# Optimization experiments

Measured on AMD Instinct MI355X. Metric: run time of the kernel, lower is better.

Reference implementation:

```python
import jax, jax.numpy as jnp
import numpy as np

B, POMO, N = 64, 200, 1000
EMB, H, D = 128, 8, 16  # head_num * qkv_dim == embedding_dim
SQRT_EMB = 11.313708498984761
CLIP = 10.0
LORA_SCALE = 16.0 / 16  # alpha / rank = 1.0


def setup_inputs() -> dict:
    key = jax.random.key(0)
    ks = jax.random.split(key, 12)
    s = 1.0 / np.sqrt(EMB)
    return {
        "encoded_nodes": jax.random.normal(ks[0], (B, N, EMB), jnp.float32),
        "encoded_q1": jax.random.normal(ks[1], (B, POMO, EMB), jnp.float32),
        "encoded_last_node": jax.random.normal(ks[2], (B, POMO, EMB), jnp.float32),
        "ninf_mask": jnp.zeros((B, POMO, N), jnp.float32),
        "Wq_first": jax.random.normal(ks[3], (H * D, EMB), jnp.float32) * s,
        "Wq_last": jax.random.normal(ks[4], (H * D, EMB), jnp.float32) * s,
        "Wk": jax.random.normal(ks[5], (H * D, EMB), jnp.float32) * s,
        "Wv": jax.random.normal(ks[6], (H * D, EMB), jnp.float32) * s,
        "Wcomb": jax.random.normal(ks[7], (EMB, H * D), jnp.float32) * s,
        "bcomb": jnp.zeros((EMB,), jnp.float32),
        "lora_q_A": jax.random.normal(ks[8], (16, EMB), jnp.float32) * s,
        "lora_q_B": jax.random.normal(ks[9], (H * D, 16), jnp.float32) * 0.01,
        "lora_c_A": jax.random.normal(ks[10], (16, H * D), jnp.float32) * s,
        "lora_c_B": jax.random.normal(ks[11], (EMB, 16), jnp.float32) * 0.01,
    }


def _heads(x):
    # [B, n, H*D] -> [B, H, n, D]
    b, n, _ = x.shape
    return x.reshape(b, n, H, D).transpose(0, 2, 1, 3)


def reference(encoded_nodes, encoded_q1, encoded_last_node, ninf_mask,
              Wq_first, Wq_last, Wk, Wv, Wcomb, bcomb,
              lora_q_A, lora_q_B, lora_c_A, lora_c_B):
    # set_kv
    k = _heads(encoded_nodes @ Wk.T)   # [B,H,N,D]
    v = _heads(encoded_nodes @ Wv.T)   # [B,H,N,D]
    # set_q1
    q_first = _heads(encoded_q1 @ Wq_first.T)  # [B,H,POMO,D]
    # forward: Wq_last + LoRA delta
    q_last_lin = encoded_last_node @ Wq_last.T \
        + ((encoded_last_node @ lora_q_A.T) @ lora_q_B.T) * LORA_SCALE
    q = q_first + _heads(q_last_lin)  # [B,H,POMO,D]
    # masked multi-head attention (rank3 mask broadcast over heads)
    score = jnp.einsum('bhnd,bhmd->bhnm', q, k) / jnp.sqrt(jnp.float32(D))
    score = score + ninf_mask[:, None, :, :]
    weights = jax.nn.softmax(score, axis=3)
    out = jnp.einsum('bhnm,bhmd->bhnd', weights, v)  # [B,H,POMO,D]
    out_concat = out.transpose(0, 2, 1, 3).reshape(encoded_q1.shape[0], -1, H * D)
    # combine + LoRA delta
    mh = out_concat @ Wcomb.T + bcomb \
        + ((out_concat @ lora_c_A.T) @ lora_c_B.T) * LORA_SCALE  # [B,POMO,EMB]
    # single-head scoring against encoder embeddings, tanh clip, mask, softmax
    score2 = jnp.einsum('bne,bme->bnm', mh, encoded_nodes) / SQRT_EMB
    score_masked = CLIP * jnp.tanh(score2) + ninf_mask
    probs = jax.nn.softmax(score_masked, axis=2)  # [B,POMO,N]
    return probs
```

## Files before the change

### kernel.cpp

```cpp
#include <hip/hip_runtime.h>
#include <hip/hip_bf16.h>


typedef _Float16 f16;
typedef _Float16 f16x2 __attribute__((ext_vector_type(2)));
typedef _Float16 f16x4 __attribute__((ext_vector_type(4)));
typedef _Float16 f16x8 __attribute__((ext_vector_type(8)));
typedef __fp16  h4   __attribute__((ext_vector_type(4)));
typedef float   f32x4 __attribute__((ext_vector_type(4)));

#define LORA_SCALE 1.0f
#define L2E 1.44269504f

__device__ __forceinline__ f16x2 pk2(f16 a, f16 b){ f16x2 r; r[0]=a; r[1]=b; return r; }

#if __has_builtin(__builtin_amdgcn_fdot2)
__device__ __forceinline__ float fdot2f(f16x2 a, f16x2 b, float c){ return __builtin_amdgcn_fdot2(a, b, c, false); }
#else
__device__ __forceinline__ float fdot2f(f16x2 a, f16x2 b, float c){ return c + (float)a[0]*(float)b[0] + (float)a[1]*(float)b[1]; }
#endif

#if __has_builtin(__builtin_amdgcn_cvt_pkrtz)
__device__ __forceinline__ f16x2 pkrtz(float a, float b){
  return __builtin_bit_cast(f16x2, __builtin_amdgcn_cvt_pkrtz(a, b));
}
#else
__device__ __forceinline__ f16x2 pkrtz(float a, float b){ return pk2((f16)a, (f16)b); }
#endif

__device__ __forceinline__ f32x4 mfma16(f16x4 a, f16x4 b, f32x4 c){
  return __builtin_amdgcn_mfma_f32_16x16x16f16(
      __builtin_bit_cast(h4, a), __builtin_bit_cast(h4, b), c, 0, 0, 0);
}

__device__ __forceinline__ float sumsq16(const f16* p){
  const f16x8* v = (const f16x8*)p;
  f16x8 a = v[0], b = v[1];
  float s = 0.f;
  s = fdot2f(pk2(a[0],a[1]), pk2(a[0],a[1]), s);
  s = fdot2f(pk2(a[2],a[3]), pk2(a[2],a[3]), s);
  s = fdot2f(pk2(a[4],a[5]), pk2(a[4],a[5]), s);
  s = fdot2f(pk2(a[6],a[7]), pk2(a[6],a[7]), s);
  s = fdot2f(pk2(b[0],b[1]), pk2(b[0],b[1]), s);
  s = fdot2f(pk2(b[2],b[3]), pk2(b[2],b[3]), s);
  s = fdot2f(pk2(b[4],b[5]), pk2(b[4],b[5]), s);
  s = fdot2f(pk2(b[6],b[7]), pk2(b[6],b[7]), s);
  return s;
}

__global__ __launch_bounds__(256) void k0_wconv(const float* __restrict__ Wk,
    const float* __restrict__ Wv, f16* __restrict__ WkvF)
{
  const int i = blockIdx.x*256 + threadIdx.x;
  const float4 v = (i < 4096) ? ((const float4*)Wk)[i] : ((const float4*)Wv)[i-4096];
  f16x2 lo = pkrtz(v.x,v.y), hi = pkrtz(v.z,v.w);
  f16x4 o = __builtin_shufflevector(lo, hi, 0, 1, 2, 3);
  *(f16x4*)(WkvF + i*4) = o;
}

#define NSTR 132
#define WSTR 136
__global__ __launch_bounds__(256) void k1_proj(const float* __restrict__ nodes,
    const f16* __restrict__ WkvF,
    f16* __restrict__ nodesT, f16* __restrict__ Kp, f16* __restrict__ Vt)
{
  __shared__ f16 lds[64*NSTR];
  __shared__ f16 wlds[16*WSTR];
  const int tid = threadIdx.x, lane = tid & 63, w = tid >> 6;
  const int b = blockIdx.y;
  const int n0 = blockIdx.x * 64;
  const int rows = min(64, 1000 - n0);
  for (int i = tid; i < rows*32; i += 256) {
    const int r = i >> 5, cq = i & 31;
    float4 v = ((const float4*)(nodes + ((size_t)b*1000 + n0 + r)*128))[cq];
    f16x2 lo = pkrtz(v.x,v.y), hi = pkrtz(v.z,v.w);
    f16x4 o = __builtin_shufflevector(lo, hi, 0, 1, 2, 3);
    *(f16x4*)(lds + r*NSTR + cq*4) = o;
    const int grow = n0 + r;
    const int t = grow >> 4, gcol = grow & 15;
    const int kk = cq >> 2, gg = cq & 3;
    f16* dstT = nodesT + (((size_t)(b*63 + t)*8 + kk)*256);
    *(f16x4*)(dstT + (gg*16 + gcol)*4) = o;
    if (grow == 999) {
      f16* d62 = nodesT + (((size_t)(b*63 + 62)*8 + kk)*256);
      #pragma unroll
      for (int cf = 8; cf < 16; ++cf) *(f16x4*)(d62 + (gg*16 + cf)*4) = o;
    }
  }
  __syncthreads();
  const int col = lane & 15, g = lane >> 4, g4 = g*4;
  const int mloc = w*16 + col;
  f16x4 nf[8];
  #pragma unroll
  for (int kk = 0; kk < 8; ++kk)
    nf[kk] = *(const f16x4*)(lds + min(mloc, rows-1)*NSTR + kk*16 + g4);
  const int wr = tid >> 4, wc = tid & 15;
  for (int ct = 0; ct < 16; ++ct) {
    __syncthreads();
    *(f16x8*)(wlds + wr*WSTR + wc*8) =
        *(const f16x8*)(WkvF + (ct*16 + wr)*128 + wc*8);
    __syncthreads();
    f16x4 wf[8];
    #pragma unroll
    for (int kk = 0; kk < 8; ++kk)
      wf[kk] = *(const f16x4*)(wlds + col*WSTR + kk*16 + g4);
    f32x4 acc = {0.f, 0.f, 0.f, 0.f};
    if (ct < 8) {
      #pragma unroll
      for (int kk = 0; kk < 8; ++kk) acc = mfma16(wf[kk], nf[kk], acc);
      if (mloc < rows) {
        const int nn = n0 + mloc;
        f16x4 ov = __builtin_shufflevector(pk2((f16)acc[0],(f16)acc[1]),
                                           pk2((f16)acc[2],(f16)acc[3]), 0,1,2,3);
        *(f16x4*)(Kp + ((size_t)(b*8+ct)*1000 + nn)*16 + g4) = ov;
      }
    } else {
      #pragma unroll
      for (int kk = 0; kk < 8; ++kk) acc = mfma16(nf[kk], wf[kk], acc);
      if (w*16 + g4 + 3 < rows) {
        const int nbase = n0 + w*16 + g4;
        f16x4 ov = __builtin_shufflevector(pk2((f16)acc[0],(f16)acc[1]),
                                           pk2((f16)acc[2],(f16)acc[3]), 0,1,2,3);
        *(f16x4*)(Vt + ((size_t)(b*8+(ct-8))*16 + col)*1000 + nbase) = ov;
      }
    }
  }
}

__global__ __launch_bounds__(256) void k1b_kmax(const f16* __restrict__ Kp,
    float* __restrict__ kmaxA)
{
  __shared__ float wmax[4];
  const int bh = blockIdx.x, tid = threadIdx.x, lane = tid & 63, w = tid >> 6;
  const f16* base = Kp + (size_t)bh*16000;
  float mx = 0.f;
  for (int n = tid; n < 1000; n += 256) mx = fmaxf(mx, sumsq16(base + n*16));
  #pragma unroll
  for (int off = 32; off; off >>= 1) mx = fmaxf(mx, __shfl_xor(mx, off, 64));
  if (lane == 0) wmax[w] = mx;
  __syncthreads();
  if (tid == 0) {
    float m = fmaxf(fmaxf(wmax[0], wmax[1]), fmaxf(wmax[2], wmax[3]));
    kmaxA[bh] = sqrtf(m);
  }
}

__global__ __launch_bounds__(256) void k2_q(const float* __restrict__ q1,
    const float* __restrict__ last, const float* __restrict__ Wqf,
    const float* __restrict__ Wql, const float* __restrict__ lqA,
    const float* __restrict__ lqB, f16* __restrict__ qF)
{
  __shared__ f16 q1r[32*128];
  __shared__ f16 lar[32*128];
  __shared__ float t16[32*16];
  const int tid = threadIdx.x;
  const int row0 = blockIdx.x * 32;
  {
    const float4* s1 = (const float4*)(q1 + (size_t)row0*128);
    const float4* s2 = (const float4*)(last + (size_t)row0*128);
    f16x2* d1 = (f16x2*)q1r; f16x2* d2 = (f16x2*)lar;
    for (int i = tid; i < 32*32; i += 256) {
      float4 v = s1[i];
      d1[2*i] = pkrtz(v.x,v.y); d1[2*i+1] = pkrtz(v.z,v.w);
      float4 u = s2[i];
      d2[2*i] = pkrtz(u.x,u.y); d2[2*i+1] = pkrtz(u.z,u.w);
    }
  }
  __syncthreads();
  for (int idx = tid; idx < 32*16; idx += 256) {
    const int r = idx >> 4, kk = idx & 15;
    const f16x8* lrow = (const f16x8*)(lar + r*128);
    const float* arow = lqA + kk*128;
    float s = 0.f;
    #pragma unroll
    for (int cc = 0; cc < 16; ++cc) {
      f16x8 a = lrow[cc];
      float4 wa = *(const float4*)(arow + cc*8);
      float4 wb = *(const float4*)(arow + cc*8 + 4);
      s = fdot2f(pk2(a[0],a[1]), pkrtz(wa.x,wa.y), s);
      s = fdot2f(pk2(a[2],a[3]), pkrtz(wa.z,wa.w), s);
      s = fdot2f(pk2(a[4],a[5]), pkrtz(wb.x,wb.y), s);
      s = fdot2f(pk2(a[6],a[7]), pkrtz(wb.z,wb.w), s);
    }
    t16[idx] = s;
  }
  __syncthreads();
  const int c = tid & 127, rg = tid >> 7, rb = rg*16;
  float acc[16];
  #pragma unroll
  for (int r = 0; r < 16; ++r) acc[r] = 0.f;
  const float* wfr = Wqf + c*128;
  const float* wlr = Wql + c*128;
  for (int c0 = 0; c0 < 128; c0 += 16) {
    float4 f0 = *(const float4*)(wfr + c0);
    float4 f1 = *(const float4*)(wfr + c0 + 4);
    float4 f2 = *(const float4*)(wfr + c0 + 8);
    float4 f3 = *(const float4*)(wfr + c0 + 12);
    f16x2 wf[8] = { pkrtz(f0.x,f0.y), pkrtz(f0.z,f0.w), pkrtz(f1.x,f1.y), pkrtz(f1.z,f1.w),
                    pkrtz(f2.x,f2.y), pkrtz(f2.z,f2.w), pkrtz(f3.x,f3.y), pkrtz(f3.z,f3.w) };
    float4 g0 = *(const float4*)(wlr + c0);
    float4 g1 = *(const float4*)(wlr + c0 + 4);
    float4 g2 = *(const float4*)(wlr + c0 + 8);
    float4 g3 = *(const float4*)(wlr + c0 + 12);
    f16x2 wl[8] = { pkrtz(g0.x,g0.y), pkrtz(g0.z,g0.w), pkrtz(g1.x,g1.y), pkrtz(g1.z,g1.w),
                    pkrtz(g2.x,g2.y), pkrtz(g2.z,g2.w), pkrtz(g3.x,g3.y), pkrtz(g3.z,g3.w) };
    #pragma unroll
    for (int r = 0; r < 16; ++r) {
      const f16x8* qp = (const f16x8*)(q1r + (rb+r)*128 + c0);
      const f16x8* lp = (const f16x8*)(lar + (rb+r)*128 + c0);
      f16x8 a0 = qp[0], a1 = qp[1], b0 = lp[0], b1 = lp[1];
      float s = acc[r];
      s = fdot2f(pk2(a0[0],a0[1]), wf[0], s);
      s = fdot2f(pk2(a0[2],a0[3]), wf[1], s);
      s = fdot2f(pk2(a0[4],a0[5]), wf[2], s);
      s = fdot2f(pk2(a0[6],a0[7]), wf[3], s);
      s = fdot2f(pk2(a1[0],a1[1]), wf[4], s);
      s = fdot2f(pk2(a1[2],a1[3]), wf[5], s);
      s = fdot2f(pk2(a1[4],a1[5]), wf[6], s);
      s = fdot2f(pk2(a1[6],a1[7]), wf[7], s);
      s = fdot2f(pk2(b0[0],b0[1]), wl[0], s);
      s = fdot2f(pk2(b0[2],b0[3]), wl[1], s);
      s = fdot2f(pk2(b0[4],b0[5]), wl[2], s);
      s = fdot2f(pk2(b0[6],b0[7]), wl[3], s);
      s = fdot2f(pk2(b1[0],b1[1]), wl[4], s);
      s = fdot2f(pk2(b1[2],b1[3]), wl[5], s);
      s = fdot2f(pk2(b1[4],b1[5]), wl[6], s);
      s = fdot2f(pk2(b1[6],b1[7]), wl[7], s);
      acc[r] = s;
    }
  }
  const float* lb = lqB + c*16;
  float lbv[16];
  #pragma unroll
  for (int i = 0; i < 16; i += 4) {
    float4 t = *(const float4*)(lb + i);
    lbv[i] = t.x; lbv[i+1] = t.y; lbv[i+2] = t.z; lbv[i+3] = t.w;
  }
  #pragma unroll
  for (int r = 0; r < 16; ++r) {
    float dl = 0.f;
    #pragma unroll
    for (int kk = 0; kk < 16; ++kk) dl += t16[(rb+r)*16 + kk] * lbv[kk];
    acc[r] += dl * LORA_SCALE;
  }
  const int h = c >> 4, d = c & 15;
  #pragma unroll
  for (int r = 0; r < 16; ++r) {
    const int grow = row0 + rb + r;
    const int b = grow / 200, m = grow % 200;
    qF[(((size_t)b*8 + h)*200 + m)*16 + d] = (f16)acc[r];
  }
}

__global__ __launch_bounds__(256) void k2b_qnorm(const f16* __restrict__ qF,
    float* __restrict__ qnA)
{
  const int idx = blockIdx.x*256 + threadIdx.x;
  qnA[idx] = sqrtf(sumsq16(qF + (size_t)idx*16));
}

#define VSTRL 516
__global__ __launch_bounds__(512) void k3_attn(const f16* __restrict__ Kp,
    const f16* __restrict__ Vt, const f16* __restrict__ qF,
    const float* __restrict__ mask, const float* __restrict__ kmaxA,
    const float* __restrict__ qnA, f16* __restrict__ Opart,
    float* __restrict__ lpart)
{
  extern __shared__ char smem[];
  f16* Kl = (f16*)smem;
  f16* Vl = (f16*)(smem + 16384);
  const int tid = threadIdx.x;
  const int lane = tid & 63, w = tid >> 6;
  const int b = blockIdx.x, h = blockIdx.y, z = blockIdx.z;
  const int bh = b*8 + h;
  {
    const int nl = tid;
    const int n = z*512 + nl;
    f16x4 v0{}, v1{}, v2{}, v3{};
    if (n < 1000) {
      const f16x4* src = (const f16x4*)(Kp + (size_t)bh*16000 + n*16);
      v0 = src[0]; v1 = src[1]; v2 = src[2]; v3 = src[3];
    }
    const int sw = (nl >> 2) & 3;
    f16* dst = Kl + nl*16;
    *(f16x4*)(dst + (0^sw)*4) = v0;
    *(f16x4*)(dst + (1^sw)*4) = v1;
    *(f16x4*)(dst + (2^sw)*4) = v2;
    *(f16x4*)(dst + (3^sw)*4) = v3;
  }
  {
    const int d = tid >> 5, c16 = (tid & 31) * 16;
    const f16* srow = Vt + (size_t)bh*16000 + d*1000;
    f16* drow = Vl + d*VSTRL + c16;
    const int nbase = z*512 + c16;
    if (nbase + 15 < 1000) {
      const f16x4* s4 = (const f16x4*)(srow + nbase);
      *(f16x4*)(drow)    = s4[0];
      *(f16x4*)(drow+4)  = s4[1];
      *(f16x4*)(drow+8)  = s4[2];
      *(f16x4*)(drow+12) = s4[3];
    } else {
      for (int j = 0; j < 16; ++j) drow[j] = (nbase+j < 1000) ? srow[nbase+j] : (f16)0;
    }
  }
  __syncthreads();

  const int col = lane & 15, g = lane >> 4, g4 = g*4;
  const int kqoff = (g ^ (col >> 2)) * 4;
  const f32x4 zero = {0.f, 0.f, 0.f, 0.f};
  const int tA = w, tB = (w + 8 < 13) ? (w + 8) : 12;
  const int mA = tA*16, mB = tB*16;
  const int mqA = min(mA + col, 199), mqB = min(mB + col, 199);
  const f16x4 qfA = *(const f16x4*)(qF + (size_t)bh*3200 + mqA*16 + g4);
  const f16x4 qfB = *(const f16x4*)(qF + (size_t)bh*3200 + mqB*16 + g4);
  const float kmx = kmaxA[bh];
  const float mbA = -kmx * qnA[bh*200 + mqA] * 0.360673760f;
  const float mbB = -kmx * qnA[bh*200 + mqB] * 0.360673760f;
  const float* mpA = mask + ((size_t)b*200 + mqA)*1000 + z*512;
  const float* mpB = mask + ((size_t)b*200 + mqB)*1000 + z*512;

  f32x4 OA = zero, OB = zero;
  float lA0=0.f, lA1=0.f, lA2=0.f, lA3=0.f;
  float lB0=0.f, lB1=0.f, lB2=0.f, lB3=0.f;
  const int NTc = 32 - z*2;
  #pragma unroll 2
  for (int t = 0; t < NTc; ++t) {
    const int nl = t*16;
    const f16x4 kf = *(const f16x4*)(Kl + (nl+col)*16 + kqoff);
    f32x4 sA = mfma16(kf, qfA, zero);
    f32x4 sB = mfma16(kf, qfB, zero);
    const float4 mkA = *(const float4*)(mpA + nl + g4);
    const float4 mkB = *(const float4*)(mpB + nl + g4);
    const float pA0 = exp2f(fmaf(sA[0], 0.360673760f, fmaf(mkA.x, L2E, mbA)));
    const float pA1 = exp2f(fmaf(sA[1], 0.360673760f, fmaf(mkA.y, L2E, mbA)));
    const float pA2 = exp2f(fmaf(sA[2], 0.360673760f, fmaf(mkA.z, L2E, mbA)));
    const float pA3 = exp2f(fmaf(sA[3], 0.360673760f, fmaf(mkA.w, L2E, mbA)));
    const float pB0 = exp2f(fmaf(sB[0], 0.360673760f, fmaf(mkB.x, L2E, mbB)));
    const float pB1 = exp2f(fmaf(sB[1], 0.360673760f, fmaf(mkB.y, L2E, mbB)));
    const float pB2 = exp2f(fmaf(sB[2], 0.360673760f, fmaf(mkB.z, L2E, mbB)));
    const float pB3 = exp2f(fmaf(sB[3], 0.360673760f, fmaf(mkB.w, L2E, mbB)));
    lA0 += pA0; lA1 += pA1; lA2 += pA2; lA3 += pA3;
    lB0 += pB0; lB1 += pB1; lB2 += pB2; lB3 += pB3;
    const f16x4 pfA = __builtin_shufflevector(pkrtz(pA0,pA1), pkrtz(pA2,pA3), 0,1,2,3);
    const f16x4 pfB = __builtin_shufflevector(pkrtz(pB0,pB1), pkrtz(pB2,pB3), 0,1,2,3);
    const f16x4 vf = *(const f16x4*)(Vl + col*VSTRL + nl + g4);
    OA = mfma16(vf, pfA, OA);
    OB = mfma16(vf, pfB, OB);
  }
  if (z == 1) {
    const int nl = 480;
    const f16x4 kf = *(const f16x4*)(Kl + (nl+col)*16 + kqoff);
    f32x4 sA = mfma16(kf, qfA, zero);
    f32x4 sB = mfma16(kf, qfB, zero);
    float pA0=0.f,pA1=0.f,pA2=0.f,pA3=0.f, pB0=0.f,pB1=0.f,pB2=0.f,pB3=0.f;
    if (g < 2) {
      const float4 mkA = *(const float4*)(mpA + nl + g4);
      const float4 mkB = *(const float4*)(mpB + nl + g4);
      pA0 = exp2f(fmaf(sA[0], 0.360673760f, fmaf(mkA.x, L2E, mbA)));
      pA1 = exp2f(fmaf(sA[1], 0.360673760f, fmaf(mkA.y, L2E, mbA)));
      pA2 = exp2f(fmaf(sA[2], 0.360673760f, fmaf(mkA.z, L2E, mbA)));
      pA3 = exp2f(fmaf(sA[3], 0.360673760f, fmaf(mkA.w, L2E, mbA)));
      pB0 = exp2f(fmaf(sB[0], 0.360673760f, fmaf(mkB.x, L2E, mbB)));
      pB1 = exp2f(fmaf(sB[1], 0.360673760f, fmaf(mkB.y, L2E, mbB)));
      pB2 = exp2f(fmaf(sB[2], 0.360673760f, fmaf(mkB.z, L2E, mbB)));
      pB3 = exp2f(fmaf(sB[3], 0.360673760f, fmaf(mkB.w, L2E, mbB)));
      lA0 += pA0; lA1 += pA1; lA2 += pA2; lA3 += pA3;
      lB0 += pB0; lB1 += pB1; lB2 += pB2; lB3 += pB3;
    }
    const f16x4 pfA = __builtin_shufflevector(pkrtz(pA0,pA1), pkrtz(pA2,pA3), 0,1,2,3);
    const f16x4 pfB = __builtin_shufflevector(pkrtz(pB0,pB1), pkrtz(pB2,pB3), 0,1,2,3);
    const f16x4 vf = *(const f16x4*)(Vl + col*VSTRL + ((g < 2) ? (nl + g4) : 0));
    OA = mfma16(vf, pfA, OA);
    OB = mfma16(vf, pfB, OB);
  }
  float lA = (lA0 + lA1) + (lA2 + lA3);
  float lB = (lB0 + lB1) + (lB2 + lB3);
  lA += __shfl_xor(lA, 16, 64); lA += __shfl_xor(lA, 32, 64);
  lB += __shfl_xor(lB, 16, 64); lB += __shfl_xor(lB, 32, 64);
  const size_t pbase = (size_t)(z*512 + bh)*200;
  if (mA + col < 200) {
    const f16x4 ov = __builtin_shufflevector(pkrtz(OA[0], OA[1]), pkrtz(OA[2], OA[3]), 0,1,2,3);
    *(f16x4*)(Opart + (pbase + mA + col)*16 + g4) = ov;
    if (g == 0) lpart[pbase + mA + col] = lA;
  }
  if (mB + col < 200) {
    const f16x4 ov = __builtin_shufflevector(pkrtz(OB[0], OB[1]), pkrtz(OB[2], OB[3]), 0,1,2,3);
    *(f16x4*)(Opart + (pbase + mB + col)*16 + g4) = ov;
    if (g == 0) lpart[pbase + mB + col] = lB;
  }
}

__global__ __launch_bounds__(256) void k3c_comb(const f16* __restrict__ Opart,
    const float* __restrict__ lpart, f16* __restrict__ ocmh)
{
  const int idx = blockIdx.x*256 + threadIdx.x;
  const int r = idx >> 2, q = idx & 3;
  const f16x4 o0 = *(const f16x4*)(Opart + (size_t)r*16 + q*4);
  const f16x4 o1 = *(const f16x4*)(Opart + ((size_t)102400 + r)*16 + q*4);
  const float l = lpart[r] + lpart[102400 + r];
  const float inv = 1.f / fmaxf(l, 1e-35f);
  const int bh = r / 200, m = r - bh*200;
  const int b = bh >> 3, hh = bh & 7;
  const float v0 = ((float)o0[0] + (float)o1[0]) * inv;
  const float v1 = ((float)o0[1] + (float)o1[1]) * inv;
  const float v2 = ((float)o0[2] + (float)o1[2]) * inv;
  const float v3 = ((float)o0[3] + (float)o1[3]) * inv;
  const f16x4 o = __builtin_shufflevector(pkrtz(v0, v1), pkrtz(v2, v3), 0, 1, 2, 3);
  *(f16x4*)(ocmh + ((size_t)(b*200 + m)*128) + hh*16 + q*4) = o;
}

__global__ __launch_bounds__(256) void k4_comb(const f16* ocF,
    const float* __restrict__ Wc, const float* __restrict__ bc,
    const float* __restrict__ lcA, const float* __restrict__ lcB,
    f16* mhF)
{
  __shared__ f16 ocr[32*128];
  __shared__ float t16[32*16];
  const int tid = threadIdx.x;
  const int row0 = blockIdx.x * 32;
  {
    const f16x8* s1 = (const f16x8*)(ocF + (size_t)row0*128);
    f16x8* d1 = (f16x8*)ocr;
    for (int i = tid; i < 512; i += 256) d1[i] = s1[i];
  }
  __syncthreads();
  for (int idx = tid; idx < 32*16; idx += 256) {
    const int r = idx >> 4, kk = idx & 15;
    const f16x8* lrow = (const f16x8*)(ocr + r*128);
    const float* arow = lcA + kk*128;
    float s = 0.f;
    #pragma unroll
    for (int cc = 0; cc < 16; ++cc) {
      f16x8 a = lrow[cc];
      float4 wa = *(const float4*)(arow + cc*8);
      float4 wb = *(const float4*)(arow + cc*8 + 4);
      s = fdot2f(pk2(a[0],a[1]), pkrtz(wa.x,wa.y), s);
      s = fdot2f(pk2(a[2],a[3]), pkrtz(wa.z,wa.w), s);
      s = fdot2f(pk2(a[4],a[5]), pkrtz(wb.x,wb.y), s);
      s = fdot2f(pk2(a[6],a[7]), pkrtz(wb.z,wb.w), s);
    }
    t16[idx] = s;
  }
  __syncthreads();
  const int c = tid & 127, rg = tid >> 7, rb = rg*16;
  float acc[16];
  const float bias = bc[c];
  #pragma unroll
  for (int r = 0; r < 16; ++r) acc[r] = bias;
  const float* wrow = Wc + c*128;
  for (int c0 = 0; c0 < 128; c0 += 16) {
    float4 w0 = *(const float4*)(wrow + c0);
    float4 w1 = *(const float4*)(wrow + c0 + 4);
    float4 w2 = *(const float4*)(wrow + c0 + 8);
    float4 w3 = *(const float4*)(wrow + c0 + 12);
    f16x2 wv[8] = { pkrtz(w0.x,w0.y), pkrtz(w0.z,w0.w), pkrtz(w1.x,w1.y), pkrtz(w1.z,w1.w),
                    pkrtz(w2.x,w2.y), pkrtz(w2.z,w2.w), pkrtz(w3.x,w3.y), pkrtz(w3.z,w3.w) };
    #pragma unroll
    for (int r = 0; r < 16; ++r) {
      const f16x8* op = (const f16x8*)(ocr + (rb+r)*128 + c0);
      f16x8 a0 = op[0], a1 = op[1];
      float s = acc[r];
      s = fdot2f(pk2(a0[0],a0[1]), wv[0], s);
      s = fdot2f(pk2(a0[2],a0[3]), wv[1], s);
      s = fdot2f(pk2(a0[4],a0[5]), wv[2], s);
      s = fdot2f(pk2(a0[6],a0[7]), wv[3], s);
      s = fdot2f(pk2(a1[0],a1[1]), wv[4], s);
      s = fdot2f(pk2(a1[2],a1[3]), wv[5], s);
      s = fdot2f(pk2(a1[4],a1[5]), wv[6], s);
      s = fdot2f(pk2(a1[6],a1[7]), wv[7], s);
      acc[r] = s;
    }
  }
  const float* lb = lcB + c*16;
  float lbv[16];
  #pragma unroll
  for (int i = 0; i < 16; i += 4) {
    float4 t = *(const float4*)(lb + i);
    lbv[i] = t.x; lbv[i+1] = t.y; lbv[i+2] = t.z; lbv[i+3] = t.w;
  }
  #pragma unroll
  for (int r = 0; r < 16; ++r) {
    float dl = 0.f;
    #pragma unroll
    for (int kk = 0; kk < 16; ++kk) dl += t16[(rb+r)*16 + kk] * lbv[kk];
    acc[r] += dl * LORA_SCALE;
  }
  #pragma unroll
  for (int r = 0; r < 16; ++r) {
    mhF[(size_t)(row0 + rb + r)*128 + c] = (f16)acc[r];
  }
}

__global__ __launch_bounds__(1024) void k5_final(const f16* __restrict__ mhF,
    const f16* __restrict__ nodesT, const float* __restrict__ mask,
    float* __restrict__ out)
{
  __shared__ float sumsA[16][16];
  __shared__ float sumsB[16][16];
  __shared__ float obuf[16][1012];
  const int tid = threadIdx.x, lane = tid & 63, w = tid >> 6;
  const int b = blockIdx.x, j = blockIdx.y;
  const int col = lane & 15, g = lane >> 4, g4 = g*4;
  const int tmA = 2*j, tmB = min(2*j + 1, 12);
  const int mA = tmA*16 + col, mB = tmB*16 + col;
  const int mqA = min(mA, 199), mqB = min(mB, 199);
  f16x4 bfA[8], bfB[8];
  {
    const f16* a = mhF + (size_t)(b*200 + mqA)*128;
    const f16* bb = mhF + (size_t)(b*200 + mqB)*128;
    #pragma unroll
    for (int kk = 0; kk < 8; ++kk) {
      bfA[kk] = *(const f16x4*)(a + kk*16 + g4);
      bfB[kk] = *(const f16x4*)(bb + kk*16 + g4);
    }
  }
  const float* mrowA = mask + (size_t)(b*200 + mqA)*1000;
  const float* mrowB = mask + (size_t)(b*200 + mqB)*1000;
  const f16* ntb = nodesT + (size_t)b*129024;
  f16x4 pfA[4], pfB[4];
  float lsumA = 0.f, lsumB = 0.f;
  #pragma unroll
  for (int i = 0; i < 4; ++i) {
    const int t = w + i*16;
    float pA0 = 0.f, pA1 = 0.f, pA2 = 0.f, pA3 = 0.f;
    float pB0 = 0.f, pB1 = 0.f, pB2 = 0.f, pB3 = 0.f;
    if (t < 63) {
      const f16* na = ntb + (size_t)t*2048;
      f32x4 accA = {0.f, 0.f, 0.f, 0.f};
      f32x4 accB = {0.f, 0.f, 0.f, 0.f};
      #pragma unroll
      for (int kk = 0; kk < 8; ++kk) {
        f16x4 af = *(const f16x4*)(na + kk*256 + lane*4);
        accA = mfma16(af, bfA[kk], accA);
        accB = mfma16(af, bfB[kk], accB);
      }
      const int n0 = t*16 + g4;
      float mkvA[4] = {0.f, 0.f, 0.f, 0.f};
      float mkvB[4] = {0.f, 0.f, 0.f, 0.f};
      if (n0 + 3 < 1000) {
        float4 mkA = *(const float4*)(mrowA + n0);
        float4 mkB = *(const float4*)(mrowB + n0);
        mkvA[0] = mkA.x; mkvA[1] = mkA.y; mkvA[2] = mkA.z; mkvA[3] = mkA.w;
        mkvB[0] = mkB.x; mkvB[1] = mkB.y; mkvB[2] = mkB.z; mkvB[3] = mkB.w;
      }
      float pvA[4], pvB[4];
      #pragma unroll
      for (int r = 0; r < 4; ++r) {
        const bool ok = (n0 + r < 1000);
        float xA = accA[r] * 0.08838834764831845f;
        float eA = exp2f(xA * 2.8853900817779268f);
        float thA = 1.f - 2.f/(eA + 1.f);
        float tA0 = exp2f((10.f*thA + mkvA[r]) * L2E);
        pvA[r] = ok ? tA0 : 0.f;
        lsumA += pvA[r];
        float xB = accB[r] * 0.08838834764831845f;
        float eB = exp2f(xB * 2.8853900817779268f);
        float thB = 1.f - 2.f/(eB + 1.f);
        float tB0 = exp2f((10.f*thB + mkvB[r]) * L2E);
        pvB[r] = ok ? tB0 : 0.f;
        lsumB += pvB[r];
      }
      pA0 = pvA[0]; pA1 = pvA[1]; pA2 = pvA[2]; pA3 = pvA[3];
      pB0 = pvB[0]; pB1 = pvB[1]; pB2 = pvB[2]; pB3 = pvB[3];
    }
    pfA[i] = __builtin_shufflevector(pkrtz(pA0, pA1), pkrtz(pA2, pA3), 0, 1, 2, 3);
    pfB[i] = __builtin_shufflevector(pkrtz(pB0, pB1), pkrtz(pB2, pB3), 0, 1, 2, 3);
  }
  lsumA += __shfl_xor(lsumA, 16, 64);
  lsumA += __shfl_xor(lsumA, 32, 64);
  lsumB += __shfl_xor(lsumB, 16, 64);
  lsumB += __shfl_xor(lsumB, 32, 64);
  if (lane < 16) { sumsA[w][lane] = lsumA; sumsB[w][lane] = lsumB; }
  __syncthreads();
  float SA = 0.f, SB = 0.f;
  #pragma unroll
  for (int ww = 0; ww < 16; ++ww) { SA += sumsA[ww][col]; SB += sumsB[ww][col]; }
  const float invA = 1.f / SA;
  const float invB = 1.f / SB;
  #pragma unroll
  for (int i = 0; i < 4; ++i) {
    const int t = w + i*16;
    if (t < 63) {
      const f16x4 pv = pfA[i];
      const int n0 = t*16 + g4;
      #pragma unroll
      for (int r = 0; r < 4; ++r) obuf[col][n0 + r] = (float)pv[r]*invA;
    }
  }
  __syncthreads();
  if (tid < 1000) {
    for (int rr = 0; rr < 16; ++rr) {
      const int m = tmA*16 + rr;
      if (m < 200) out[((size_t)b*200 + m)*1000 + tid] = obuf[rr][tid];
    }
  }
  __syncthreads();
  if (tmB != tmA) {
    #pragma unroll
    for (int i = 0; i < 4; ++i) {
      const int t = w + i*16;
      if (t < 63) {
        const f16x4 pv = pfB[i];
        const int n0 = t*16 + g4;
        #pragma unroll
        for (int r = 0; r < 4; ++r) obuf[col][n0 + r] = (float)pv[r]*invB;
      }
    }
    __syncthreads();
    if (tid < 1000) {
      for (int rr = 0; rr < 16; ++rr) {
        const int m = tmB*16 + rr;
        if (m < 200) out[((size_t)b*200 + m)*1000 + tid] = obuf[rr][tid];
      }
    }
  }
}

extern "C" void kernel_launch(void* const* d_in, const int* in_sizes, int n_in,
                              void* d_out, int out_size, void* d_ws, size_t ws_size,
                              hipStream_t stream)
{
  (void)in_sizes; (void)n_in; (void)out_size; (void)ws_size;
  const float* nodes = (const float*)d_in[0];
  const float* q1    = (const float*)d_in[1];
  const float* last  = (const float*)d_in[2];
  const float* mask  = (const float*)d_in[3];
  const float* Wqf   = (const float*)d_in[4];
  const float* Wql   = (const float*)d_in[5];
  const float* Wk    = (const float*)d_in[6];
  const float* Wv    = (const float*)d_in[7];
  const float* Wc    = (const float*)d_in[8];
  const float* bc    = (const float*)d_in[9];
  const float* lqA   = (const float*)d_in[10];
  const float* lqB   = (const float*)d_in[11];
  const float* lcA   = (const float*)d_in[12];
  const float* lcB   = (const float*)d_in[13];
  float* out = (float*)d_out;
  char* ws = (char*)d_ws;
  f16* Kp      = (f16*)(ws + 16384000);
  f16* Vt      = (f16*)(ws + 32768000);
  f16* qF      = (f16*)(ws + 49152000);
  f16* ocmh    = (f16*)(ws + 52428800);
  f16* WkvF    = (f16*)(ws + 55705600);
  float* kmaxA = (float*)(ws + 55771136);
  float* qnA   = (float*)(ws + 55773184);
  f16* OpartF  = (f16*)(ws + 56182784);
  float* lpart = (float*)(ws + 62736384);
  f16* nodesT  = (f16*)(ws + 63555584);

  k0_wconv<<<dim3(32), 256, 0, stream>>>(Wk, Wv, WkvF);
  k1_proj<<<dim3(16, 64), 256, 0, stream>>>(nodes, WkvF, nodesT, Kp, Vt);
  k1b_kmax<<<dim3(512), 256, 0, stream>>>(Kp, kmaxA);
  k2_q<<<dim3(400), 256, 0, stream>>>(q1, last, Wqf, Wql, lqA, lqB, qF);
  k2b_qnorm<<<dim3(400), 256, 0, stream>>>(qF, qnA);
  k3_attn<<<dim3(64, 8, 2), 512, 32896, stream>>>(Kp, Vt, qF, mask, kmaxA, qnA, OpartF, lpart);
  k3c_comb<<<dim3(1600), 256, 0, stream>>>(OpartF, lpart, ocmh);
  k4_comb<<<dim3(400), 256, 0, stream>>>(ocmh, Wc, bc, lcA, lcB, ocmh);
  k5_final<<<dim3(64, 7), 1024, 0, stream>>>(ocmh, nodesT, mask, out);
}
```

Measured before the change: 195.4 us.

## Fuse weight conversion into projection, merge norm kernels, pad K LDS layout

Drops the separate weight-conversion kernel: k1_proj now reads fp32 Wk/Wv directly and converts them while staging into LDS. The K-max and q-norm kernels become one launch. In attention, the XOR-swizzled K LDS layout is replaced by a padded row stride of 20 halves, and the main loop unroll goes from 2 to 4. Together these cut two kernel launches, at the cost of every projection block redundantly converting the weights, more LDS per attention block, and a possible change in bank-conflict behaviour.

```diff
diff --git a/kernel.cpp b/kernel.cpp
--- a/kernel.cpp
+++ b/kernel.cpp
@@ -48,20 +48,10 @@
   return s;
 }
 
-__global__ __launch_bounds__(256) void k0_wconv(const float* __restrict__ Wk,
-    const float* __restrict__ Wv, f16* __restrict__ WkvF)
-{
-  const int i = blockIdx.x*256 + threadIdx.x;
-  const float4 v = (i < 4096) ? ((const float4*)Wk)[i] : ((const float4*)Wv)[i-4096];
-  f16x2 lo = pkrtz(v.x,v.y), hi = pkrtz(v.z,v.w);
-  f16x4 o = __builtin_shufflevector(lo, hi, 0, 1, 2, 3);
-  *(f16x4*)(WkvF + i*4) = o;
-}
-
 #define NSTR 132
 #define WSTR 136
 __global__ __launch_bounds__(256) void k1_proj(const float* __restrict__ nodes,
-    const f16* __restrict__ WkvF,
+    const float* __restrict__ Wk, const float* __restrict__ Wv,
     f16* __restrict__ nodesT, f16* __restrict__ Kp, f16* __restrict__ Vt)
 {
   __shared__ f16 lds[64*NSTR];
@@ -97,8 +87,16 @@
   const int wr = tid >> 4, wc = tid & 15;
   for (int ct = 0; ct < 16; ++ct) {
     __syncthreads();
-    *(f16x8*)(wlds + wr*WSTR + wc*8) =
-        *(const f16x8*)(WkvF + (ct*16 + wr)*128 + wc*8);
+    {
+      const int r = ct*16 + wr;
+      const float* src = (r < 128) ? (Wk + (size_t)r*128) : (Wv + (size_t)(r-128)*128);
+      float4 a = *(const float4*)(src + wc*8);
+      float4 bb = *(const float4*)(src + wc*8 + 4);
+      *(f16x4*)(wlds + wr*WSTR + wc*8) =
+          __builtin_shufflevector(pkrtz(a.x,a.y), pkrtz(a.z,a.w), 0,1,2,3);
+      *(f16x4*)(wlds + wr*WSTR + wc*8 + 4) =
+          __builtin_shufflevector(pkrtz(bb.x,bb.y), pkrtz(bb.z,bb.w), 0,1,2,3);
+    }
     __syncthreads();
     f16x4 wf[8];
     #pragma unroll
@@ -127,21 +125,26 @@
   }
 }
 
-__global__ __launch_bounds__(256) void k1b_kmax(const f16* __restrict__ Kp,
-    float* __restrict__ kmaxA)
-{
-  __shared__ float wmax[4];
-  const int bh = blockIdx.x, tid = threadIdx.x, lane = tid & 63, w = tid >> 6;
-  const f16* base = Kp + (size_t)bh*16000;
-  float mx = 0.f;
-  for (int n = tid; n < 1000; n += 256) mx = fmaxf(mx, sumsq16(base + n*16));
-  #pragma unroll
-  for (int off = 32; off; off >>= 1) mx = fmaxf(mx, __shfl_xor(mx, off, 64));
-  if (lane == 0) wmax[w] = mx;
-  __syncthreads();
-  if (tid == 0) {
-    float m = fmaxf(fmaxf(wmax[0], wmax[1]), fmaxf(wmax[2], wmax[3]));
-    kmaxA[bh] = sqrtf(m);
+__global__ __launch_bounds__(256) void kb_norms(const f16* __restrict__ Kp,
+    const f16* __restrict__ qF, float* __restrict__ kmaxA, float* __restrict__ qnA)
+{
+  if (blockIdx.x < 512) {
+    __shared__ float wmax[4];
+    const int bh = blockIdx.x, tid = threadIdx.x, lane = tid & 63, w = tid >> 6;
+    const f16* base = Kp + (size_t)bh*16000;
+    float mx = 0.f;
+    for (int n = tid; n < 1000; n += 256) mx = fmaxf(mx, sumsq16(base + n*16));
+    #pragma unroll
+    for (int off = 32; off; off >>= 1) mx = fmaxf(mx, __shfl_xor(mx, off, 64));
+    if (lane == 0) wmax[w] = mx;
+    __syncthreads();
+    if (tid == 0) {
+      float m = fmaxf(fmaxf(wmax[0], wmax[1]), fmaxf(wmax[2], wmax[3]));
+      kmaxA[bh] = sqrtf(m);
+    }
+  } else {
+    const int idx = (blockIdx.x - 512)*256 + threadIdx.x;
+    qnA[idx] = sqrtf(sumsq16(qF + (size_t)idx*16));
   }
 }
 
@@ -252,13 +255,7 @@
   }
 }
 
-__global__ __launch_bounds__(256) void k2b_qnorm(const f16* __restrict__ qF,
-    float* __restrict__ qnA)
-{
-  const int idx = blockIdx.x*256 + threadIdx.x;
-  qnA[idx] = sqrtf(sumsq16(qF + (size_t)idx*16));
-}
-
+#define KSTR 20
 #define VSTRL 516
 __global__ __launch_bounds__(512) void k3_attn(const f16* __restrict__ Kp,
     const f16* __restrict__ Vt, const f16* __restrict__ qF,
@@ -268,7 +265,7 @@
 {
   extern __shared__ char smem[];
   f16* Kl = (f16*)smem;
-  f16* Vl = (f16*)(smem + 16384);
+  f16* Vl = (f16*)(smem + 20480);
   const int tid = threadIdx.x;
   const int lane = tid & 63, w = tid >> 6;
   const int b = blockIdx.x, h = blockIdx.y, z = blockIdx.z;
@@ -281,12 +278,11 @@
       const f16x4* src = (const f16x4*)(Kp + (size_t)bh*16000 + n*16);
       v0 = src[0]; v1 = src[1]; v2 = src[2]; v3 = src[3];
     }
-    const int sw = (nl >> 2) & 3;
-    f16* dst = Kl + nl*16;
-    *(f16x4*)(dst + (0^sw)*4) = v0;
-    *(f16x4*)(dst + (1^sw)*4) = v1;
-    *(f16x4*)(dst + (2^sw)*4) = v2;
-    *(f16x4*)(dst + (3^sw)*4) = v3;
+    f16* dst = Kl + nl*KSTR;
+    *(f16x4*)(dst)    = v0;
+    *(f16x4*)(dst+4)  = v1;
+    *(f16x4*)(dst+8)  = v2;
+    *(f16x4*)(dst+12) = v3;
   }
   {
     const int d = tid >> 5, c16 = (tid & 31) * 16;
@@ -306,7 +302,6 @@
   __syncthreads();
 
   const int col = lane & 15, g = lane >> 4, g4 = g*4;
-  const int kqoff = (g ^ (col >> 2)) * 4;
   const f32x4 zero = {0.f, 0.f, 0.f, 0.f};
   const int tA = w, tB = (w + 8 < 13) ? (w + 8) : 12;
   const int mA = tA*16, mB = tB*16;
@@ -323,10 +318,10 @@
   float lA0=0.f, lA1=0.f, lA2=0.f, lA3=0.f;
   float lB0=0.f, lB1=0.f, lB2=0.f, lB3=0.f;
   const int NTc = 32 - z*2;
-  #pragma unroll 2
+  #pragma unroll 4
   for (int t = 0; t < NTc; ++t) {
     const int nl = t*16;
-    const f16x4 kf = *(const f16x4*)(Kl + (nl+col)*16 + kqoff);
+    const f16x4 kf = *(const f16x4*)(Kl + (nl+col)*KSTR + g4);
     f32x4 sA = mfma16(kf, qfA, zero);
     f32x4 sB = mfma16(kf, qfB, zero);
     const float4 mkA = *(const float4*)(mpA + nl + g4);
@@ -349,7 +344,7 @@
   }
   if (z == 1) {
     const int nl = 480;
-    const f16x4 kf = *(const f16x4*)(Kl + (nl+col)*16 + kqoff);
+    const f16x4 kf = *(const f16x4*)(Kl + (nl+col)*KSTR + g4);
     f32x4 sA = mfma16(kf, qfA, zero);
     f32x4 sB = mfma16(kf, qfB, zero);
     float pA0=0.f,pA1=0.f,pA2=0.f,pA3=0.f, pB0=0.f,pB1=0.f,pB2=0.f,pB3=0.f;
@@ -641,19 +636,16 @@
   f16* Vt      = (f16*)(ws + 32768000);
   f16* qF      = (f16*)(ws + 49152000);
   f16* ocmh    = (f16*)(ws + 52428800);
-  f16* WkvF    = (f16*)(ws + 55705600);
   float* kmaxA = (float*)(ws + 55771136);
   float* qnA   = (float*)(ws + 55773184);
   f16* OpartF  = (f16*)(ws + 56182784);
   float* lpart = (float*)(ws + 62736384);
   f16* nodesT  = (f16*)(ws + 63555584);
 
-  k0_wconv<<<dim3(32), 256, 0, stream>>>(Wk, Wv, WkvF);
-  k1_proj<<<dim3(16, 64), 256, 0, stream>>>(nodes, WkvF, nodesT, Kp, Vt);
-  k1b_kmax<<<dim3(512), 256, 0, stream>>>(Kp, kmaxA);
+  k1_proj<<<dim3(16, 64), 256, 0, stream>>>(nodes, Wk, Wv, nodesT, Kp, Vt);
   k2_q<<<dim3(400), 256, 0, stream>>>(q1, last, Wqf, Wql, lqA, lqB, qF);
-  k2b_qnorm<<<dim3(400), 256, 0, stream>>>(qF, qnA);
-  k3_attn<<<dim3(64, 8, 2), 512, 32896, stream>>>(Kp, Vt, qF, mask, kmaxA, qnA, OpartF, lpart);
+  kb_norms<<<dim3(912), 256, 0, stream>>>(Kp, qF, kmaxA, qnA);
+  k3_attn<<<dim3(64, 8, 2), 512, 36992, stream>>>(Kp, Vt, qF, mask, kmaxA, qnA, OpartF, lpart);
   k3c_comb<<<dim3(1600), 256, 0, stream>>>(OpartF, lpart, ocmh);
   k4_comb<<<dim3(400), 256, 0, stream>>>(ocmh, Wc, bc, lcA, lcB, ocmh);
   k5_final<<<dim3(64, 7), 1024, 0, stream>>>(ocmh, nodesT, mask, out);
```

Result: faster. 188.6 us (-3.5%).
